# Optimization experiments

Measured on AMD Instinct MI355X. Metric: run time of the kernel, lower is better.

The kernel has to match this reference:

```python
import jax, jax.numpy as jnp
import numpy as np


def setup_inputs() -> dict:
    key = jax.random.key(0)
    x = jax.random.normal(key, (16, 3, 512, 512), dtype=jnp.float32)
    return {"x": x}


def reference(x):
    # x: [B, C, H, W] with H, W even.
    B, C, H, W = x.shape
    # --- single-level 2D Haar DWT (pywt 'haar' convention) ---
    # View each 2x2 block: a=top-left, b=top-right, c=bottom-left, d=bottom-right.
    blocks = x.reshape(B, C, H // 2, 2, W // 2, 2)
    a = blocks[:, :, :, 0, :, 0]
    b = blocks[:, :, :, 0, :, 1]
    c = blocks[:, :, :, 1, :, 0]
    d = blocks[:, :, :, 1, :, 1]
    half = jnp.asarray(0.5, x.dtype)
    LL = (a + b + c + d) * half  # cA
    LH = (a + b - c - d) * half  # cH (horizontal detail)
    HL = (a - b + c - d) * half  # cV (vertical detail)
    HH = (a - b - c + d) * half  # cD (diagonal detail)
    # [B, C, 4, H/2, W/2]
    sub = jnp.stack([LL, LH, HL, HH], axis=2)
    # Bilinear upsample back to (H, W); jax.image bilinear uses half-pixel
    # centers, matching F.interpolate(mode='bilinear', align_corners=False).
    up = jax.image.resize(sub, (B, C, 4, H, W), method="bilinear")
    # IG: original channel resized to its own size -> identity under this mode.
    bands = jnp.concatenate([x[:, :, None], up], axis=2)  # [B, C, 5, H, W]
    return bands.reshape(B, 5 * C, H, W)
```

## Files before the change

kernel.cpp:

```cpp
#include <hip/hip_runtime.h>

#define BC   48
#define CNUM 3
#define HF   512
#define WF   512
#define HH   256
#define WH   256
#define TILE 16

__device__ __forceinline__ float4 mix13(const float4 a, const float4 b) {
    float4 r;
    r.x = fmaf(0.25f, a.x, 0.75f * b.x);
    r.y = fmaf(0.25f, a.y, 0.75f * b.y);
    r.z = fmaf(0.25f, a.z, 0.75f * b.z);
    r.w = fmaf(0.25f, a.w, 0.75f * b.w);
    return r;
}

__device__ __forceinline__ float4 mix31(const float4 a, const float4 b) {
    float4 r;
    r.x = fmaf(0.75f, a.x, 0.25f * b.x);
    r.y = fmaf(0.75f, a.y, 0.25f * b.y);
    r.z = fmaf(0.75f, a.z, 0.25f * b.z);
    r.w = fmaf(0.75f, a.w, 0.25f * b.w);
    return r;
}

__device__ __forceinline__ void store2(float* p, float a, float b) {
    float2 v; v.x = a; v.y = b;
    *reinterpret_cast<float2*>(p) = v;
}

__global__ __launch_bounds__(256) void wavelet_kernel(const float* __restrict__ x,
                                                      float* __restrict__ out) {
    __shared__ float4 coef[TILE + 2][TILE + 3];

    const int tx = threadIdx.x;
    const int ty = threadIdx.y;
    const int k0 = blockIdx.y * TILE;
    const int l0 = blockIdx.x * TILE;
    const int bc = blockIdx.z;
    const int b  = bc / CNUM;
    const int c  = bc - b * CNUM;

    const float* __restrict__ xin = x + (size_t)bc * (HF * WF);

    const int t = ty * TILE + tx;
    for (int i = t; i < (TILE + 2) * (TILE + 2); i += 256) {
        const int ry = i / (TILE + 2);
        const int rx = i - ry * (TILE + 2);
        int k = k0 + ry - 1; k = k < 0 ? 0 : (k > HH - 1 ? HH - 1 : k);
        int l = l0 + rx - 1; l = l < 0 ? 0 : (l > WH - 1 ? WH - 1 : l);
        const float* p = xin + (2 * k) * WF + 2 * l;
        const float2 top = *reinterpret_cast<const float2*>(p);
        const float2 bot = *reinterpret_cast<const float2*>(p + WF);
        const float a = top.x, bb = top.y, cc = bot.x, dd = bot.y;
        float4 v;
        v.x = (a + bb + cc + dd) * 0.5f;
        v.y = (a + bb - cc - dd) * 0.5f;
        v.z = (a - bb + cc - dd) * 0.5f;
        v.w = (a - bb - cc + dd) * 0.5f;
        coef[ry][rx] = v;
    }
    __syncthreads();

    const int k = k0 + ty;
    const int l = l0 + tx;

    const float4 c00 = coef[ty][tx],     c01 = coef[ty][tx + 1],     c02 = coef[ty][tx + 2];
    const float4 c10 = coef[ty + 1][tx], c11 = coef[ty + 1][tx + 1], c12 = coef[ty + 1][tx + 2];
    const float4 c20 = coef[ty + 2][tx], c21 = coef[ty + 2][tx + 1], c22 = coef[ty + 2][tx + 2];

    const float4 h0r0 = mix13(c00, c01), h1r0 = mix31(c01, c02);
    const float4 h0r1 = mix13(c10, c11), h1r1 = mix31(c11, c12);
    const float4 h0r2 = mix13(c20, c21), h1r2 = mix31(c21, c22);

    const float4 v00 = mix13(h0r0, h0r1);
    const float4 v01 = mix13(h1r0, h1r1);
    const float4 v10 = mix31(h0r1, h0r2);
    const float4 v11 = mix31(h1r1, h1r2);

    const int y0 = 2 * k;
    const int x0 = 2 * l;
    float* __restrict__ outp = out + (size_t)(b * 15 + c * 5) * HF * WF;

    {
        const float* p = xin + y0 * WF + x0;
        const float2 t0 = *reinterpret_cast<const float2*>(p);
        const float2 t1 = *reinterpret_cast<const float2*>(p + WF);
        store2(outp + (size_t)y0 * WF + x0, t0.x, t0.y);
        store2(outp + (size_t)(y0 + 1) * WF + x0, t1.x, t1.y);
    }
    {
        float* o = outp + (size_t)1 * HF * WF;
        store2(o + (size_t)y0 * WF + x0, v00.x, v01.x);
        store2(o + (size_t)(y0 + 1) * WF + x0, v10.x, v11.x);
    }
    {
        float* o = outp + (size_t)2 * HF * WF;
        store2(o + (size_t)y0 * WF + x0, v00.y, v01.y);
        store2(o + (size_t)(y0 + 1) * WF + x0, v10.y, v11.y);
    }
    {
        float* o = outp + (size_t)3 * HF * WF;
        store2(o + (size_t)y0 * WF + x0, v00.z, v01.z);
        store2(o + (size_t)(y0 + 1) * WF + x0, v10.z, v11.z);
    }
    {
        float* o = outp + (size_t)4 * HF * WF;
        store2(o + (size_t)y0 * WF + x0, v00.w, v01.w);
        store2(o + (size_t)(y0 + 1) * WF + x0, v10.w, v11.w);
    }
}

extern "C" void kernel_launch(void* const* d_in, const int* in_sizes, int n_in,
                              void* d_out, int out_size, void* d_ws, size_t ws_size,
                              hipStream_t stream) {
    const float* x = (const float*)d_in[0];
    float* out = (float*)d_out;
    dim3 grid(WH / TILE, HH / TILE, BC);
    dim3 block(TILE, TILE);
    hipLaunchKernelGGL(wavelet_kernel, grid, block, 0, stream, x, out);
}
```

Before: 286.8 us.

## Process two coarse columns per thread with 16-byte nontemporal stores

Each thread now handles two half-resolution columns, so every output row segment is written as a float4 instead of a float2. The tile widens to 32 columns, which shrinks the halo overhead per output, and all stores become nontemporal to avoid polluting cache with write-only data. The cost is more registers per thread and half as many blocks.

```diff
diff --git a/kernel.cpp b/kernel.cpp
--- a/kernel.cpp
+++ b/kernel.cpp
@@ -1,116 +1,91 @@
 #include <hip/hip_runtime.h>
 
 #define BC   48
-#define CNUM 3
 #define HF   512
 #define WF   512
 #define HH   256
 #define WH   256
-#define TILE 16
+#define TK   16
+#define TL   32
+#define HW   (HF * WF)
 
-__device__ __forceinline__ float4 mix13(const float4 a, const float4 b) {
-    float4 r;
-    r.x = fmaf(0.25f, a.x, 0.75f * b.x);
-    r.y = fmaf(0.25f, a.y, 0.75f * b.y);
-    r.z = fmaf(0.25f, a.z, 0.75f * b.z);
-    r.w = fmaf(0.25f, a.w, 0.75f * b.w);
-    return r;
-}
-
-__device__ __forceinline__ float4 mix31(const float4 a, const float4 b) {
-    float4 r;
-    r.x = fmaf(0.75f, a.x, 0.25f * b.x);
-    r.y = fmaf(0.75f, a.y, 0.25f * b.y);
-    r.z = fmaf(0.75f, a.z, 0.25f * b.z);
-    r.w = fmaf(0.75f, a.w, 0.25f * b.w);
-    return r;
-}
-
-__device__ __forceinline__ void store2(float* p, float a, float b) {
-    float2 v; v.x = a; v.y = b;
-    *reinterpret_cast<float2*>(p) = v;
-}
+typedef float v4 __attribute__((ext_vector_type(4)));
+typedef float v2 __attribute__((ext_vector_type(2)));
 
 __global__ __launch_bounds__(256) void wavelet_kernel(const float* __restrict__ x,
                                                       float* __restrict__ out) {
-    __shared__ float4 coef[TILE + 2][TILE + 3];
+    __shared__ v4 coef[TK + 2][TL + 3];
 
     const int tx = threadIdx.x;
     const int ty = threadIdx.y;
-    const int k0 = blockIdx.y * TILE;
-    const int l0 = blockIdx.x * TILE;
+    const int k0 = blockIdx.y * TK;
+    const int l0 = blockIdx.x * TL;
     const int bc = blockIdx.z;
-    const int b  = bc / CNUM;
-    const int c  = bc - b * CNUM;
 
-    const float* __restrict__ xin = x + (size_t)bc * (HF * WF);
+    const float* __restrict__ xin = x + (size_t)bc * HW;
 
-    const int t = ty * TILE + tx;
-    for (int i = t; i < (TILE + 2) * (TILE + 2); i += 256) {
-        const int ry = i / (TILE + 2);
-        const int rx = i - ry * (TILE + 2);
+    const int t = ty * 16 + tx;
+    for (int i = t; i < (TK + 2) * (TL + 2); i += 256) {
+        const int ry = i / (TL + 2);
+        const int rx = i - ry * (TL + 2);
         int k = k0 + ry - 1; k = k < 0 ? 0 : (k > HH - 1 ? HH - 1 : k);
         int l = l0 + rx - 1; l = l < 0 ? 0 : (l > WH - 1 ? WH - 1 : l);
-        const float* p = xin + (2 * k) * WF + 2 * l;
-        const float2 top = *reinterpret_cast<const float2*>(p);
-        const float2 bot = *reinterpret_cast<const float2*>(p + WF);
-        const float a = top.x, bb = top.y, cc = bot.x, dd = bot.y;
-        float4 v;
-        v.x = (a + bb + cc + dd) * 0.5f;
-        v.y = (a + bb - cc - dd) * 0.5f;
-        v.z = (a - bb + cc - dd) * 0.5f;
-        v.w = (a - bb - cc + dd) * 0.5f;
+        const float* p = xin + (size_t)(2 * k) * WF + 2 * l;
+        const v2 top = *reinterpret_cast<const v2*>(p);
+        const v2 bot = *reinterpret_cast<const v2*>(p + WF);
+        const float a = top.x, b = top.y, c = bot.x, d = bot.y;
+        v4 v;
+        v.x = (a + b + c + d) * 0.5f;
+        v.y = (a + b - c - d) * 0.5f;
+        v.z = (a - b + c - d) * 0.5f;
+        v.w = (a - b - c + d) * 0.5f;
         coef[ry][rx] = v;
     }
     __syncthreads();
 
-    const int k = k0 + ty;
-    const int l = l0 + tx;
+    v4 hr[3][4];
+#pragma unroll
+    for (int r = 0; r < 3; ++r) {
+        const v4 A = coef[ty + r][2 * tx];
+        const v4 B = coef[ty + r][2 * tx + 1];
+        const v4 C = coef[ty + r][2 * tx + 2];
+        const v4 D = coef[ty + r][2 * tx + 3];
+        hr[r][0] = A * 0.25f + B * 0.75f;
+        hr[r][1] = B * 0.75f + C * 0.25f;
+        hr[r][2] = B * 0.25f + C * 0.75f;
+        hr[r][3] = C * 0.75f + D * 0.25f;
+    }
+    v4 ve[4], vo[4];
+#pragma unroll
+    for (int j = 0; j < 4; ++j) {
+        ve[j] = hr[0][j] * 0.25f + hr[1][j] * 0.75f;
+        vo[j] = hr[1][j] * 0.75f + hr[2][j] * 0.25f;
+    }
 
-    const float4 c00 = coef[ty][tx],     c01 = coef[ty][tx + 1],     c02 = coef[ty][tx + 2];
-    const float4 c10 = coef[ty + 1][tx], c11 = coef[ty + 1][tx + 1], c12 = coef[ty + 1][tx + 2];
-    const float4 c20 = coef[ty + 2][tx], c21 = coef[ty + 2][tx + 1], c22 = coef[ty + 2][tx + 2];
-
-    const float4 h0r0 = mix13(c00, c01), h1r0 = mix31(c01, c02);
-    const float4 h0r1 = mix13(c10, c11), h1r1 = mix31(c11, c12);
-    const float4 h0r2 = mix13(c20, c21), h1r2 = mix31(c21, c22);
-
-    const float4 v00 = mix13(h0r0, h0r1);
-    const float4 v01 = mix13(h1r0, h1r1);
-    const float4 v10 = mix31(h0r1, h0r2);
-    const float4 v11 = mix31(h1r1, h1r2);
-
-    const int y0 = 2 * k;
-    const int x0 = 2 * l;
-    float* __restrict__ outp = out + (size_t)(b * 15 + c * 5) * HF * WF;
+    const int y0 = 2 * (k0 + ty);
+    const int x0 = 2 * l0 + 4 * tx;
+    float* __restrict__ outp = out + (size_t)bc * 5 * HW;
 
     {
-        const float* p = xin + y0 * WF + x0;
-        const float2 t0 = *reinterpret_cast<const float2*>(p);
-        const float2 t1 = *reinterpret_cast<const float2*>(p + WF);
-        store2(outp + (size_t)y0 * WF + x0, t0.x, t0.y);
-        store2(outp + (size_t)(y0 + 1) * WF + x0, t1.x, t1.y);
+        const v4 t0 = *reinterpret_cast<const v4*>(xin + (size_t)y0 * WF + x0);
+        const v4 t1 = *reinterpret_cast<const v4*>(xin + (size_t)(y0 + 1) * WF + x0);
+        __builtin_nontemporal_store(t0, reinterpret_cast<v4*>(outp + (size_t)y0 * WF + x0));
+        __builtin_nontemporal_store(t1, reinterpret_cast<v4*>(outp + (size_t)(y0 + 1) * WF + x0));
     }
-    {
-        float* o = outp + (size_t)1 * HF * WF;
-        store2(o + (size_t)y0 * WF + x0, v00.x, v01.x);
-        store2(o + (size_t)(y0 + 1) * WF + x0, v10.x, v11.x);
+#define STORE_BAND(BIDX, COMP)                                                         \
+    {                                                                                  \
+        v4 e, o;                                                                       \
+        e.x = ve[0].COMP; e.y = ve[1].COMP; e.z = ve[2].COMP; e.w = ve[3].COMP;        \
+        o.x = vo[0].COMP; o.y = vo[1].COMP; o.z = vo[2].COMP; o.w = vo[3].COMP;        \
+        float* ob = outp + (size_t)BIDX * HW;                                          \
+        __builtin_nontemporal_store(e, reinterpret_cast<v4*>(ob + (size_t)y0 * WF + x0)); \
+        __builtin_nontemporal_store(o, reinterpret_cast<v4*>(ob + (size_t)(y0 + 1) * WF + x0)); \
     }
-    {
-        float* o = outp + (size_t)2 * HF * WF;
-        store2(o + (size_t)y0 * WF + x0, v00.y, v01.y);
-        store2(o + (size_t)(y0 + 1) * WF + x0, v10.y, v11.y);
-    }
-    {
-        float* o = outp + (size_t)3 * HF * WF;
-        store2(o + (size_t)y0 * WF + x0, v00.z, v01.z);
-        store2(o + (size_t)(y0 + 1) * WF + x0, v10.z, v11.z);
-    }
-    {
-        float* o = outp + (size_t)4 * HF * WF;
-        store2(o + (size_t)y0 * WF + x0, v00.w, v01.w);
-        store2(o + (size_t)(y0 + 1) * WF + x0, v10.w, v11.w);
-    }
+    STORE_BAND(1, x)
+    STORE_BAND(2, y)
+    STORE_BAND(3, z)
+    STORE_BAND(4, w)
+#undef STORE_BAND
 }
 
 extern "C" void kernel_launch(void* const* d_in, const int* in_sizes, int n_in,
@@ -118,7 +93,7 @@
                               hipStream_t stream) {
     const float* x = (const float*)d_in[0];
     float* out = (float*)d_out;
-    dim3 grid(WH / TILE, HH / TILE, BC);
-    dim3 block(TILE, TILE);
+    dim3 grid(WH / TL, HH / TK, BC);
+    dim3 block(16, 16);
     hipLaunchKernelGGL(wavelet_kernel, grid, block, 0, stream, x, out);
 }
```

New measurement: 280.0 us. -2.3%, faster.
